# Performance work log

Measured on AMD Instinct MI355X. Metric: run time of the kernel, lower is better.

## Reference

```python
import jax, jax.numpy as jnp
import numpy as np

# Sizes (see shape_source): node irreps 32x0e + 16x1o, edge SH 1x1o,
# messages after concat/filter = 48x0e + 48x1o, MLP 16->64->64->96,
# final equivariant Linear -> 32x0e + 16x1o.
N, E = 50000, 800000
S_IN, V_IN, INV = 32, 16, 16
S_MSG, V_MSG = S_IN + V_IN, S_IN + V_IN  # 48, 48
NFAC = S_MSG + V_MSG                      # 96
S_OUT, V_OUT = 32, 16
SQRT3 = 3.0 ** 0.5


def setup_inputs() -> dict:
    key = jax.random.key(0)
    ks = jax.random.split(key, 12)
    return {
        "edge_src": jax.random.randint(ks[0], (E,), 0, N),
        "edge_dst": jax.random.randint(ks[1], (E,), 0, N),
        "edge_weight_cutoff": jax.random.uniform(ks[2], (E,), dtype=jnp.float32),
        "edge_inv": jax.random.normal(ks[3], (E, INV), dtype=jnp.float32),
        "node_scalars": jax.random.normal(ks[4], (N, S_IN), dtype=jnp.float32),
        "node_vectors": jax.random.normal(ks[5], (N, V_IN, 3), dtype=jnp.float32),
        "edge_sh_vec": jax.random.normal(ks[6], (E, 1, 3), dtype=jnp.float32),
        "W0": jax.random.normal(ks[7], (INV, 64), dtype=jnp.float32),
        "W1": jax.random.normal(ks[8], (64, 64), dtype=jnp.float32),
        "W2": jax.random.normal(ks[9], (64, NFAC), dtype=jnp.float32),
        "WL_s": jax.random.normal(ks[10], (S_MSG, S_OUT), dtype=jnp.float32),
        "WL_v": jax.random.normal(ks[11], (V_MSG, V_OUT), dtype=jnp.float32),
    }


def reference(edge_src, edge_dst, edge_weight_cutoff, edge_inv,
              node_scalars, node_vectors, edge_sh_vec,
              W0, W1, W2, WL_s, WL_v):
    # gather source-node features per edge
    src_s = node_scalars[edge_src]            # [E, 32]
    src_v = node_vectors[edge_src]            # [E, 16, 3]
    ev = edge_sh_vec[:, 0, :]                 # [E, 3] equivariant edge vector (1o)

    # equivariant tensor product (component-normalized CG paths):
    #   0e x 1o -> 1o : scalar * vector
    tp_v = src_s[:, :, None] * edge_sh_vec    # [E, 32, 3]
    #   1o x 1o -> 0e : dot / sqrt(3)   (1e, 2e outputs dropped by the output-irreps filter)
    tp_s = jnp.einsum('eci,ei->ec', src_v, ev) / SQRT3  # [E, 16]

    # concatenate with gathered node features and regroup by irrep
    msg_s = jnp.concatenate([tp_s, src_s], axis=-1)     # [E, 48] (0e block)
    msg_v = jnp.concatenate([tp_v, src_v], axis=1)      # [E, 48, 3] (1o block)

    # edge-conditioned gating MLP on invariant edge features (e3nn-normalized)
    h = jax.nn.silu(edge_inv @ W0 / jnp.sqrt(jnp.float32(INV)))
    h = jax.nn.silu(h @ W1 / jnp.sqrt(jnp.float32(64)))
    fac = h @ W2 / jnp.sqrt(jnp.float32(64))            # [E, 96]

    # elementwise tensor product with scalar factors + smooth cutoff
    g = fac * edge_weight_cutoff[:, None]
    msg_s = msg_s * g[:, :S_MSG]
    msg_v = msg_v * g[:, S_MSG:, None]

    # scatter-sum messages into destination nodes
    out_s = jax.ops.segment_sum(msg_s, edge_dst, num_segments=N)  # [N, 48]
    out_v = jax.ops.segment_sum(msg_v, edge_dst, num_segments=N)  # [N, 48, 3]

    # equivariant Linear to irreps_node_output (fan-in normalized)
    y_s = out_s @ WL_s / jnp.sqrt(jnp.float32(S_MSG))                       # [N, 32]
    y_v = jnp.einsum('eci,co->eoi', out_v, WL_v) / jnp.sqrt(jnp.float32(V_MSG))  # [N, 16, 3]

    # return as contiguous IrrepsArray storage [N, 32 + 16*3]
    return jnp.concatenate([y_s, y_v.reshape(y_v.shape[0], -1)], axis=-1)
```

## Files before the change

kernel.cpp:

```cpp
#include <hip/hip_runtime.h>
#include <hip/hip_fp16.h>
#include <math.h>

constexpr int S_IN = 32, V_IN = 16, INVD = 16;
constexpr int S_MSG = S_IN + V_IN;
constexpr int V_MSG = S_IN + V_IN;
constexpr int NFAC  = S_MSG + V_MSG;
constexpr int S_OUT = 32, V_OUT = 16;
constexpr int OUT_PER_NODE = S_OUT + V_OUT * 3;
constexpr float ISQRT3 = 0.57735026918962576f;
constexpr float ISQ48  = 0.14433756729740643f;

constexpr int PW0 = 0, PW1 = 2560, PW2 = 7168, PWL = 14080, PWTOT = 17536;

typedef _Float16 f16x8 __attribute__((ext_vector_type(8)));
typedef __attribute__((ext_vector_type(4))) float f32x4;

__device__ __forceinline__ float silu_f(float x) {
    return x / (1.0f + __expf(-x));
}
__device__ __forceinline__ unsigned int hpack2(float a, float b) {
    __half2 h = __floats2half2_rn(a, b);
    return *reinterpret_cast<unsigned int*>(&h);
}
__device__ __forceinline__ unsigned short f2h(float f) {
    __half h = __float2half_rn(f);
    return __half_as_ushort(h);
}
__device__ __forceinline__ float h2f(unsigned short u) {
    return __half2float(__ushort_as_half(u));
}
__device__ __forceinline__ void ld4h(const unsigned short* p, float f[4]) {
    uint2 v = *reinterpret_cast<const uint2*>(p);
    f[0] = h2f((unsigned short)(v.x & 0xffffu));
    f[1] = h2f((unsigned short)(v.x >> 16));
    f[2] = h2f((unsigned short)(v.y & 0xffffu));
    f[3] = h2f((unsigned short)(v.y >> 16));
}

__global__ __launch_bounds__(256) void hist_prep(
    const int* __restrict__ edst, int* __restrict__ deg, int E,
    const float* __restrict__ W0, const float* __restrict__ W1,
    const float* __restrict__ W2, const float* __restrict__ WLs,
    const float* __restrict__ WLv,
    const float* __restrict__ ns, const float* __restrict__ nv,
    unsigned short* __restrict__ pW,
    unsigned short* __restrict__ pNS,
    unsigned short* __restrict__ pNV,
    int Nn)
{
    int i = blockIdx.x * 256 + threadIdx.x;
    if (i < E) atomicAdd(&deg[edst[i]], 1);

    int nNS = Nn * 4;
    int nNV = Nn * 6;
    if (i < PWTOT) {
        float v = 0.0f;
        if (i < PW1) {
            int j = i / 40, k = i - 40 * j;
            if (k < INVD) v = W0[k * 64 + j];
        } else if (i < PW2) {
            int t = i - PW1; int j = t / 72, k = t - 72 * j;
            if (k < 64) v = W1[k * 64 + j];
        } else if (i < PWL) {
            int t = i - PW2; int j = t / 72, k = t - 72 * j;
            if (k < 64) v = W2[k * 96 + j];
        } else {
            int t = i - PWL; int j = t / 72, k = t - 72 * j;
            if (k < 48) v = (j < 32) ? WLs[k * S_OUT + j] : WLv[k * V_OUT + (j - 32)];
        }
        pW[i] = f2h(v);
    } else if (i < PWTOT + nNS) {
        int g = i - PWTOT;
        const float4* s4 = reinterpret_cast<const float4*>(ns + (size_t)g * 8);
        float4 a = s4[0], b = s4[1];
        *reinterpret_cast<uint4*>(pNS + (size_t)g * 8) =
            make_uint4(hpack2(a.x, a.y), hpack2(a.z, a.w), hpack2(b.x, b.y), hpack2(b.z, b.w));
    } else if (i < PWTOT + nNS + nNV) {
        int g = i - PWTOT - nNS;
        const float4* s4 = reinterpret_cast<const float4*>(nv + (size_t)g * 8);
        float4 a = s4[0], b = s4[1];
        *reinterpret_cast<uint4*>(pNV + (size_t)g * 8) =
            make_uint4(hpack2(a.x, a.y), hpack2(a.z, a.w), hpack2(b.x, b.y), hpack2(b.z, b.w));
    }
}

__global__ __launch_bounds__(256) void scanA(
    const int* __restrict__ deg, int* __restrict__ bsum, int Nn)
{
    __shared__ int sh[256];
    int i = blockIdx.x * 256 + threadIdx.x;
    sh[threadIdx.x] = (i < Nn) ? deg[i] : 0;
    __syncthreads();
    for (int o = 128; o > 0; o >>= 1) {
        if (threadIdx.x < o) sh[threadIdx.x] += sh[threadIdx.x + o];
        __syncthreads();
    }
    if (threadIdx.x == 0) bsum[blockIdx.x] = sh[0];
}

__global__ __launch_bounds__(1024) void scanB(int* __restrict__ bsum, int nb)
{
    __shared__ int sh[1024];
    int t = threadIdx.x;
    sh[t] = (t < nb) ? bsum[t] : 0;
    __syncthreads();
    for (int o = 1; o < 1024; o <<= 1) {
        int v = (t >= o) ? sh[t - o] : 0;
        __syncthreads();
        sh[t] += v;
        __syncthreads();
    }
    if (t < nb) bsum[t] = (t > 0) ? sh[t - 1] : 0;
}

__global__ __launch_bounds__(256) void scanC(
    const int* __restrict__ deg, const int* __restrict__ bsum,
    int* __restrict__ offs, int* __restrict__ cursor, int Nn, int E)
{
    __shared__ int sh[256];
    int i = blockIdx.x * 256 + threadIdx.x;
    int t = threadIdx.x;
    int v = (i < Nn) ? deg[i] : 0;
    sh[t] = v;
    __syncthreads();
    for (int o = 1; o < 256; o <<= 1) {
        int u = (t >= o) ? sh[t - o] : 0;
        __syncthreads();
        sh[t] += u;
        __syncthreads();
    }
    int excl = sh[t] - v + bsum[blockIdx.x];
    if (i < Nn) { offs[i] = excl; cursor[i] = excl; }
    if (i == Nn - 1) offs[Nn] = E;
}

__global__ __launch_bounds__(256) void scatter_permute(
    const int*   __restrict__ edst,
    const int*   __restrict__ esrc,
    const float* __restrict__ ecut,
    const float* __restrict__ esh,
    const float* __restrict__ einv,
    int* __restrict__ cursor,
    uint4* __restrict__ pedge,
    int E)
{
    int e = blockIdx.x * 256 + threadIdx.x;
    if (e >= E) return;
    int d = edst[e];
    int pos = atomicAdd(&cursor[d], 1);

    const float4* xr = reinterpret_cast<const float4*>(einv + (size_t)e * INVD);
    float4 a = xr[0], b = xr[1], c = xr[2], f = xr[3];
    uint4 r0 = make_uint4(hpack2(a.x, a.y), hpack2(a.z, a.w), hpack2(b.x, b.y), hpack2(b.z, b.w));
    uint4 r1 = make_uint4(hpack2(c.x, c.y), hpack2(c.z, c.w), hpack2(f.x, f.y), hpack2(f.z, f.w));
    uint4 r2 = make_uint4(__float_as_uint(ecut[e]),
                          __float_as_uint(esh[(size_t)e * 3 + 0]),
                          __float_as_uint(esh[(size_t)e * 3 + 1]),
                          __float_as_uint(esh[(size_t)e * 3 + 2]));
    uint4 r3 = make_uint4((unsigned int)esrc[e], (unsigned int)d, 0u, 0u);

    uint4* dst = pedge + (size_t)pos * 4;
    dst[0] = r0; dst[1] = r1; dst[2] = r2; dst[3] = r3;
}

__global__ __launch_bounds__(256, 3) void edge_mega(
    const uint4* __restrict__ pedge,
    const unsigned short* __restrict__ pW,
    const unsigned short* __restrict__ pNS,
    const unsigned short* __restrict__ pNV,
    float* __restrict__ out,
    int E)
{
    __shared__ __align__(16) unsigned char smem[53760];

    unsigned short* sW0T = (unsigned short*)(smem + 0);
    unsigned short* sW1T = (unsigned short*)(smem + 5120);
    unsigned short* act0 = (unsigned short*)(smem + 14336);
    unsigned short* act1 = (unsigned short*)(smem + 32768);
    unsigned short* sWLT = (unsigned short*)(smem + 5120);
    unsigned short* M    = (unsigned short*)(smem + 14336);
    unsigned short* Fns  = (unsigned short*)(smem + 32768);
    int*            sdst = (int*)(smem + 43008);
    unsigned short* Fnv0 = (unsigned short*)(smem + 43520);
    unsigned short* Fnv1 = (unsigned short*)(smem + 48640);
    unsigned short* Fnv2 = (unsigned short*)(smem + 0);
    float*          redf = (float*)smem;

    const int tid = threadIdx.x;
    const int pbase = blockIdx.x * 128;
    const int p1 = E;

    const int lane = tid & 63;
    const int w    = tid >> 6;
    const int lr   = lane & 15;
    const int lg   = lane >> 4;
    const int eb0  = w * 32 + lr;
    const int eb1  = eb0 + 16;
    const int pA   = pbase + eb0;
    const int pB   = pbase + eb1;

    const uint4 rA2 = pedge[(size_t)(pA < p1 ? pA : p1 - 1) * 4 + 2];
    const uint4 rB2 = pedge[(size_t)(pB < p1 ? pB : p1 - 1) * 4 + 2];
    const float cutA = __uint_as_float(rA2.x);
    const float ev0a = __uint_as_float(rA2.y), ev1a = __uint_as_float(rA2.z), ev2a = __uint_as_float(rA2.w);
    const float cutB = __uint_as_float(rB2.x);
    const float ev0b = __uint_as_float(rB2.y), ev1b = __uint_as_float(rB2.z), ev2b = __uint_as_float(rB2.w);

    const int t2 = tid >> 1, half = tid & 1;
    int dS;
    uint4 pf0, pf1, pf2, pf3, pf4, pf5;
    {
        int pS = pbase + t2; if (pS >= p1) pS = p1 - 1;
        uint4 r3 = pedge[(size_t)pS * 4 + 3];
        int sS = (int)r3.x;
        dS = (int)r3.y;
        if (half == 0) {
            const uint4* nr = reinterpret_cast<const uint4*>(pNS + (size_t)sS * 32);
            pf0 = nr[0]; pf1 = nr[1]; pf2 = nr[2]; pf3 = nr[3];
        } else {
            const uint4* vr = reinterpret_cast<const uint4*>(pNV + (size_t)sS * 48);
            pf0 = vr[0]; pf1 = vr[1]; pf2 = vr[2]; pf3 = vr[3]; pf4 = vr[4]; pf5 = vr[5];
        }
    }

    const uint4* wsrc = reinterpret_cast<const uint4*>(pW);

    {
        uint4* s4 = reinterpret_cast<uint4*>(smem);
        #pragma unroll 2
        for (int i = tid; i < 896; i += 256) s4[i] = wsrc[i];
    }
    if (tid < 128) {
        int p = pbase + tid; if (p >= p1) p = p1 - 1;
        const uint4* rec = pedge + (size_t)p * 4;
        uint4 r0 = rec[0], r1 = rec[1];
        uint4* r4 = reinterpret_cast<uint4*>(&act0[tid * 72]);
        r4[0] = r0;
        r4[1] = r1;
        r4[2] = make_uint4(0u, 0u, 0u, 0u);
        r4[3] = make_uint4(0u, 0u, 0u, 0u);
    }
    __syncthreads();

    const f32x4 zero4 = {0.f, 0.f, 0.f, 0.f};

    {
        f16x8 b0 = *(const f16x8*)&act0[eb0 * 72 + lg * 8];
        f16x8 b1 = *(const f16x8*)&act0[eb1 * 72 + lg * 8];
        #pragma unroll
        for (int jt = 0; jt < 4; jt++) {
            f16x8 a = *(const f16x8*)&sW0T[(jt * 16 + lr) * 40 + lg * 8];
            f32x4 d0 = __builtin_amdgcn_mfma_f32_16x16x32_f16(a, b0, zero4, 0, 0, 0);
            f32x4 d1 = __builtin_amdgcn_mfma_f32_16x16x32_f16(a, b1, zero4, 0, 0, 0);
            unsigned int u0 = hpack2(silu_f(d0[0] * 0.25f), silu_f(d0[1] * 0.25f));
            unsigned int u1 = hpack2(silu_f(d0[2] * 0.25f), silu_f(d0[3] * 0.25f));
            *(uint2*)&act1[eb0 * 72 + jt * 16 + lg * 4] = make_uint2(u0, u1);
            u0 = hpack2(silu_f(d1[0] * 0.25f), silu_f(d1[1] * 0.25f));
            u1 = hpack2(silu_f(d1[2] * 0.25f), silu_f(d1[3] * 0.25f));
            *(uint2*)&act1[eb1 * 72 + jt * 16 + lg * 4] = make_uint2(u0, u1);
        }
    }

    {
        f16x8 b00 = *(const f16x8*)&act1[eb0 * 72 +      lg * 8];
        f16x8 b01 = *(const f16x8*)&act1[eb0 * 72 + 32 + lg * 8];
        f16x8 b10 = *(const f16x8*)&act1[eb1 * 72 +      lg * 8];
        f16x8 b11 = *(const f16x8*)&act1[eb1 * 72 + 32 + lg * 8];
        #pragma unroll
        for (int jt = 0; jt < 4; jt++) {
            f16x8 a0 = *(const f16x8*)&sW1T[(jt * 16 + lr) * 72 +      lg * 8];
            f16x8 a1 = *(const f16x8*)&sW1T[(jt * 16 + lr) * 72 + 32 + lg * 8];
            f32x4 d0 = __builtin_amdgcn_mfma_f32_16x16x32_f16(a0, b00, zero4, 0, 0, 0);
            d0 = __builtin_amdgcn_mfma_f32_16x16x32_f16(a1, b01, d0, 0, 0, 0);
            f32x4 d1 = __builtin_amdgcn_mfma_f32_16x16x32_f16(a0, b10, zero4, 0, 0, 0);
            d1 = __builtin_amdgcn_mfma_f32_16x16x32_f16(a1, b11, d1, 0, 0, 0);
            unsigned int u0 = hpack2(silu_f(d0[0] * 0.125f), silu_f(d0[1] * 0.125f));
            unsigned int u1 = hpack2(silu_f(d0[2] * 0.125f), silu_f(d0[3] * 0.125f));
            *(uint2*)&act0[eb0 * 72 + jt * 16 + lg * 4] = make_uint2(u0, u1);
            u0 = hpack2(silu_f(d1[0] * 0.125f), silu_f(d1[1] * 0.125f));
            u1 = hpack2(silu_f(d1[2] * 0.125f), silu_f(d1[3] * 0.125f));
            *(uint2*)&act0[eb1 * 72 + jt * 16 + lg * 4] = make_uint2(u0, u1);
        }
    }

    __syncthreads();
    {
        uint4* a14 = reinterpret_cast<uint4*>(act1);
        const uint4* w2s = wsrc + 896;
        #pragma unroll 2
        for (int i = tid; i < 864; i += 256) a14[i] = w2s[i];
    }
    __syncthreads();

    float fac0[6][4], fac1[6][4];
    {
        f16x8 b00 = *(const f16x8*)&act0[eb0 * 72 +      lg * 8];
        f16x8 b01 = *(const f16x8*)&act0[eb0 * 72 + 32 + lg * 8];
        f16x8 b10 = *(const f16x8*)&act0[eb1 * 72 +      lg * 8];
        f16x8 b11 = *(const f16x8*)&act0[eb1 * 72 + 32 + lg * 8];
        float K0 = cutA * 0.125f * ISQ48;
        float K1 = cutB * 0.125f * ISQ48;
        #pragma unroll
        for (int jt = 0; jt < 6; jt++) {
            f16x8 a0 = *(const f16x8*)&act1[(jt * 16 + lr) * 72 +      lg * 8];
            f16x8 a1 = *(const f16x8*)&act1[(jt * 16 + lr) * 72 + 32 + lg * 8];
            f32x4 d0 = __builtin_amdgcn_mfma_f32_16x16x32_f16(a0, b00, zero4, 0, 0, 0);
            d0 = __builtin_amdgcn_mfma_f32_16x16x32_f16(a1, b01, d0, 0, 0, 0);
            f32x4 d1 = __builtin_amdgcn_mfma_f32_16x16x32_f16(a0, b10, zero4, 0, 0, 0);
            d1 = __builtin_amdgcn_mfma_f32_16x16x32_f16(a1, b11, d1, 0, 0, 0);
            float s0 = (jt == 0) ? K0 * ISQRT3 : K0;
            float s1 = (jt == 0) ? K1 * ISQRT3 : K1;
            #pragma unroll
            for (int q = 0; q < 4; q++) {
                fac0[jt][q] = d0[q] * s0;
                fac1[jt][q] = d1[q] * s1;
            }
        }
    }
    __syncthreads();

    {
        if (half == 0) {
            uint4* d4 = reinterpret_cast<uint4*>(&Fns[t2 * 40]);
            d4[0] = pf0; d4[1] = pf1;
            uint4* d4b = reinterpret_cast<uint4*>(&Fns[t2 * 40 + 16]);
            d4b[0] = pf2; d4b[1] = pf3;
        } else {
            unsigned int wb[24];
            wb[0]=pf0.x; wb[1]=pf0.y; wb[2]=pf0.z; wb[3]=pf0.w;
            wb[4]=pf1.x; wb[5]=pf1.y; wb[6]=pf1.z; wb[7]=pf1.w;
            wb[8]=pf2.x; wb[9]=pf2.y; wb[10]=pf2.z; wb[11]=pf2.w;
            wb[12]=pf3.x; wb[13]=pf3.y; wb[14]=pf3.z; wb[15]=pf3.w;
            wb[16]=pf4.x; wb[17]=pf4.y; wb[18]=pf4.z; wb[19]=pf4.w;
            wb[20]=pf5.x; wb[21]=pf5.y; wb[22]=pf5.z; wb[23]=pf5.w;
            #pragma unroll
            for (int i = 0; i < 3; i++) {
                unsigned short* FnvI = (i == 0) ? Fnv0 : ((i == 1) ? Fnv1 : Fnv2);
                unsigned int ow[8];
                #pragma unroll
                for (int wd = 0; wd < 8; wd++) {
                    int kLo = 6 * wd + i;
                    int kHi = 6 * wd + 3 + i;
                    unsigned int lo = (kLo & 1) ? (wb[kLo >> 1] >> 16) : (wb[kLo >> 1] & 0xffffu);
                    unsigned int hi = (kHi & 1) ? (wb[kHi >> 1] >> 16) : (wb[kHi >> 1] & 0xffffu);
                    ow[wd] = lo | (hi << 16);
                }
                uint2* d2 = reinterpret_cast<uint2*>(&FnvI[t2 * 20]);
                d2[0] = make_uint2(ow[0], ow[1]);
                d2[1] = make_uint2(ow[2], ow[3]);
                d2[2] = make_uint2(ow[4], ow[5]);
                d2[3] = make_uint2(ow[6], ow[7]);
            }
        }
        uint4* wl4 = reinterpret_cast<uint4*>(sWLT);
        const uint4* wls = wsrc + 896 + 864;
        #pragma unroll 2
        for (int i = tid; i < 432; i += 256) wl4[i] = wls[i];
    }
    __syncthreads();

    float fvA[3][4], fvB[3][4];
    float fsA[2][4], fsB[2][4];
    #pragma unroll
    for (int i = 0; i < 3; i++) {
        const unsigned short* FnvI = (i == 0) ? Fnv0 : ((i == 1) ? Fnv1 : Fnv2);
        ld4h(&FnvI[eb0 * 20 + lg * 4], fvA[i]);
        ld4h(&FnvI[eb1 * 20 + lg * 4], fvB[i]);
    }
    #pragma unroll
    for (int jt = 0; jt < 2; jt++) {
        ld4h(&Fns[eb0 * 40 + jt * 16 + lg * 4], fsA[jt]);
        ld4h(&Fns[eb1 * 40 + jt * 16 + lg * 4], fsB[jt]);
    }

    {
        float vA[4], vB[4];
        #pragma unroll
        for (int q = 0; q < 4; q++) {
            float fa = fvA[0][q] * ev0a + fvA[1][q] * ev1a + fvA[2][q] * ev2a;
            float fb = fvB[0][q] * ev0b + fvB[1][q] * ev1b + fvB[2][q] * ev2b;
            vA[q] = fa * fac0[0][q];
            vB[q] = fb * fac1[0][q];
        }
        *(uint2*)&M[eb0 * 72 + lg * 4] = make_uint2(hpack2(vA[0], vA[1]), hpack2(vA[2], vA[3]));
        *(uint2*)&M[eb1 * 72 + lg * 4] = make_uint2(hpack2(vB[0], vB[1]), hpack2(vB[2], vB[3]));
    }
    #pragma unroll
    for (int jt = 1; jt < 3; jt++) {
        int c0 = jt * 16 + lg * 4;
        float vA[4], vB[4];
        #pragma unroll
        for (int q = 0; q < 4; q++) {
            vA[q] = fsA[jt - 1][q] * fac0[jt][q];
            vB[q] = fsB[jt - 1][q] * fac1[jt][q];
        }
        *(uint2*)&M[eb0 * 72 + c0] = make_uint2(hpack2(vA[0], vA[1]), hpack2(vA[2], vA[3]));
        *(uint2*)&M[eb1 * 72 + c0] = make_uint2(hpack2(vB[0], vB[1]), hpack2(vB[2], vB[3]));
    }
    *(uint2*)&M[eb0 * 72 + 48 + lg * 4] = make_uint2(0u, 0u);
    *(uint2*)&M[eb1 * 72 + 48 + lg * 4] = make_uint2(0u, 0u);

    f32x4 accS[2][2] = {{zero4, zero4}, {zero4, zero4}};
    #pragma unroll
    for (int kt = 0; kt < 2; kt++) {
        f16x8 b0 = *(const f16x8*)&M[eb0 * 72 + kt * 32 + lg * 8];
        f16x8 b1 = *(const f16x8*)&M[eb1 * 72 + kt * 32 + lg * 8];
        #pragma unroll
        for (int ot = 0; ot < 2; ot++) {
            f16x8 a = *(const f16x8*)&sWLT[(ot * 16 + lr) * 72 + kt * 32 + lg * 8];
            accS[0][ot] = __builtin_amdgcn_mfma_f32_16x16x32_f16(a, b0, accS[0][ot], 0, 0, 0);
            accS[1][ot] = __builtin_amdgcn_mfma_f32_16x16x32_f16(a, b1, accS[1][ot], 0, 0, 0);
        }
    }

    #pragma unroll
    for (int jt = 0; jt < 2; jt++) {
        int c0 = jt * 16 + lg * 4;
        float vA[4], vB[4];
        #pragma unroll
        for (int q = 0; q < 4; q++) {
            vA[q] = fsA[jt][q] * fac0[3 + jt][q];
            vB[q] = fsB[jt][q] * fac1[3 + jt][q];
        }
        *(uint2*)&M[eb0 * 72 + c0] = make_uint2(hpack2(vA[0], vA[1]), hpack2(vA[2], vA[3]));
        *(uint2*)&M[eb1 * 72 + c0] = make_uint2(hpack2(vB[0], vB[1]), hpack2(vB[2], vB[3]));
    }
    f32x4 t1A = zero4, t1B = zero4;
    {
        f16x8 b0 = *(const f16x8*)&M[eb0 * 72 + lg * 8];
        f16x8 b1 = *(const f16x8*)&M[eb1 * 72 + lg * 8];
        f16x8 a  = *(const f16x8*)&sWLT[(32 + lr) * 72 + lg * 8];
        t1A = __builtin_amdgcn_mfma_f32_16x16x32_f16(a, b0, t1A, 0, 0, 0);
        t1B = __builtin_amdgcn_mfma_f32_16x16x32_f16(a, b1, t1B, 0, 0, 0);
    }

    float yvA[4][3], yvB[4][3];
    *(uint2*)&M[eb0 * 72 + 16 + lg * 4] = make_uint2(0u, 0u);
    *(uint2*)&M[eb1 * 72 + 16 + lg * 4] = make_uint2(0u, 0u);
    #pragma unroll
    for (int i = 0; i < 3; i++) {
        float vA[4], vB[4];
        #pragma unroll
        for (int q = 0; q < 4; q++) {
            vA[q] = fvA[i][q] * fac0[5][q];
            vB[q] = fvB[i][q] * fac1[5][q];
        }
        *(uint2*)&M[eb0 * 72 + lg * 4] = make_uint2(hpack2(vA[0], vA[1]), hpack2(vA[2], vA[3]));
        *(uint2*)&M[eb1 * 72 + lg * 4] = make_uint2(hpack2(vB[0], vB[1]), hpack2(vB[2], vB[3]));

        f32x4 t2A = zero4, t2B = zero4;
        f16x8 b0 = *(const f16x8*)&M[eb0 * 72 + lg * 8];
        f16x8 b1 = *(const f16x8*)&M[eb1 * 72 + lg * 8];
        f16x8 a  = *(const f16x8*)&sWLT[(32 + lr) * 72 + 32 + lg * 8];
        t2A = __builtin_amdgcn_mfma_f32_16x16x32_f16(a, b0, t2A, 0, 0, 0);
        t2B = __builtin_amdgcn_mfma_f32_16x16x32_f16(a, b1, t2B, 0, 0, 0);

        float evA = (i == 0) ? ev0a : ((i == 1) ? ev1a : ev2a);
        float evB = (i == 0) ? ev0b : ((i == 1) ? ev1b : ev2b);
        #pragma unroll
        for (int q = 0; q < 4; q++) {
            yvA[q][i] = fmaf(evA, t1A[q], t2A[q]);
            yvB[q][i] = fmaf(evB, t1B[q], t2B[q]);
        }
    }

    __syncthreads();

    if (half == 0) sdst[t2] = dS;

    {
        bool okA = (pA < p1), okB = (pB < p1);
        #pragma unroll
        for (int ot = 0; ot < 2; ot++) {
            *(f32x4*)&redf[eb0 * 84 + ot * 16 + lg * 4] = okA ? accS[0][ot] : zero4;
            *(f32x4*)&redf[eb1 * 84 + ot * 16 + lg * 4] = okB ? accS[1][ot] : zero4;
        }
        #pragma unroll
        for (int q = 0; q < 4; q++) {
            int m = lg * 4 + q;
            #pragma unroll
            for (int i = 0; i < 3; i++) {
                redf[eb0 * 84 + 32 + 3 * m + i] = okA ? yvA[q][i] : 0.0f;
                redf[eb1 * 84 + 32 + 3 * m + i] = okB ? yvB[q][i] : 0.0f;
            }
        }
    }
    __syncthreads();

    {
        int base = w * 32;
        int cur = sdst[base];
        float s0 = 0.0f, s1 = 0.0f;
        for (int r = 0; r < 32; r++) {
            int d = sdst[base + r];
            if (d != cur) {
                atomicAdd(&out[(size_t)cur * OUT_PER_NODE + lane], s0);
                if (lane < 16) atomicAdd(&out[(size_t)cur * OUT_PER_NODE + 64 + lane], s1);
                s0 = 0.0f; s1 = 0.0f; cur = d;
            }
            s0 += redf[(base + r) * 84 + lane];
            if (lane < 16) s1 += redf[(base + r) * 84 + 64 + lane];
        }
        atomicAdd(&out[(size_t)cur * OUT_PER_NODE + lane], s0);
        if (lane < 16) atomicAdd(&out[(size_t)cur * OUT_PER_NODE + 64 + lane], s1);
    }
}

extern "C" void kernel_launch(void* const* d_in, const int* in_sizes, int n_in,
                              void* d_out, int out_size, void* d_ws, size_t ws_size,
                              hipStream_t stream) {
    const int*   esrc = (const int*)  d_in[0];
    const int*   edst = (const int*)  d_in[1];
    const float* ecut = (const float*)d_in[2];
    const float* einv = (const float*)d_in[3];
    const float* ns   = (const float*)d_in[4];
    const float* nv   = (const float*)d_in[5];
    const float* esh  = (const float*)d_in[6];
    const float* W0   = (const float*)d_in[7];
    const float* W1   = (const float*)d_in[8];
    const float* W2   = (const float*)d_in[9];
    const float* WLs  = (const float*)d_in[10];
    const float* WLv  = (const float*)d_in[11];
    float* out = (float*)d_out;

    const int E  = in_sizes[0];
    const int Nn = in_sizes[4] / S_IN;
    const int nb = (Nn + 255) / 256;

    size_t int_bytes = (((size_t)(3 * Nn + 1 + nb)) * sizeof(int) + 255) & ~(size_t)255;
    size_t pe_bytes  = ((size_t)E * 64 + 255) & ~(size_t)255;
    size_t pw_bytes  = ((size_t)PWTOT * 2 + 255) & ~(size_t)255;
    size_t ns_bytes  = ((size_t)Nn * 32 * 2 + 255) & ~(size_t)255;
    size_t nv_bytes  = ((size_t)Nn * 48 * 2 + 255) & ~(size_t)255;
    size_t fixed = int_bytes + pe_bytes + pw_bytes + ns_bytes + nv_bytes;

    int eblocks = (E + 255) / 256;

    hipMemsetAsync(out, 0, (size_t)Nn * OUT_PER_NODE * sizeof(float), stream);

    if (ws_size < fixed) return;

    int*            deg    = (int*)d_ws;
    int*            offs   = deg + Nn;
    int*            cursor = offs + Nn + 1;
    int*            bsum   = cursor + Nn;
    uint4*          pedge  = (uint4*)((char*)d_ws + int_bytes);
    unsigned short* pW     = (unsigned short*)((char*)d_ws + int_bytes + pe_bytes);
    unsigned short* pNS    = (unsigned short*)((char*)d_ws + int_bytes + pe_bytes + pw_bytes);
    unsigned short* pNV    = (unsigned short*)((char*)d_ws + int_bytes + pe_bytes + pw_bytes + ns_bytes);

    hipMemsetAsync(deg, 0, (size_t)Nn * sizeof(int), stream);

    int ptotal = PWTOT + Nn * 4 + Nn * 6;
    int hp_blocks = max(eblocks, (ptotal + 255) / 256);
    hist_prep<<<hp_blocks, 256, 0, stream>>>(edst, deg, E, W0, W1, W2, WLs, WLv,
                                             ns, nv, pW, pNS, pNV, Nn);
    scanA<<<nb, 256, 0, stream>>>(deg, bsum, Nn);
    scanB<<<1, 1024, 0, stream>>>(bsum, nb);
    scanC<<<nb, 256, 0, stream>>>(deg, bsum, offs, cursor, Nn, E);
    scatter_permute<<<eblocks, 256, 0, stream>>>(edst, esrc, ecut, esh, einv,
                                                 cursor, pedge, E);

    int mblocks = (E + 127) / 128;
    edge_mega<<<mblocks, 256, 0, stream>>>(pedge, pW, pNS, pNV, out, E);
}
```

Before: 214.3 us.

## Compress edge records to 48 bytes and use packed fp16 gating multiplies

Shrinks the permuted per-edge record from 64 to 48 bytes by storing the cutoff and edge vector as fp16 and putting src/dst in the third uint4. This cuts the bytes written by the scatter kernel and read by the edge megakernel. The gating multiplies now run as packed half2 multiplies on raw fp16 registers rather than unpacking to float, and silu uses a hardware reciprocal. The cost is lower precision for the cutoff, the edge vector and the gated products.

```diff
diff --git a/kernel.cpp b/kernel.cpp
--- a/kernel.cpp
+++ b/kernel.cpp
@@ -17,7 +17,7 @@
 typedef __attribute__((ext_vector_type(4))) float f32x4;
 
 __device__ __forceinline__ float silu_f(float x) {
-    return x / (1.0f + __expf(-x));
+    return x * __builtin_amdgcn_rcpf(1.0f + __expf(-x));
 }
 __device__ __forceinline__ unsigned int hpack2(float a, float b) {
     __half2 h = __floats2half2_rn(a, b);
@@ -30,12 +30,17 @@
 __device__ __forceinline__ float h2f(unsigned short u) {
     return __half2float(__ushort_as_half(u));
 }
-__device__ __forceinline__ void ld4h(const unsigned short* p, float f[4]) {
-    uint2 v = *reinterpret_cast<const uint2*>(p);
-    f[0] = h2f((unsigned short)(v.x & 0xffffu));
-    f[1] = h2f((unsigned short)(v.x >> 16));
-    f[2] = h2f((unsigned short)(v.y & 0xffffu));
-    f[3] = h2f((unsigned short)(v.y >> 16));
+__device__ __forceinline__ float lo16f(unsigned int u) { return h2f((unsigned short)(u & 0xffffu)); }
+__device__ __forceinline__ float hi16f(unsigned int u) { return h2f((unsigned short)(u >> 16)); }
+__device__ __forceinline__ unsigned int pkmul(unsigned int a, unsigned int b) {
+    __half2 ha = *reinterpret_cast<__half2*>(&a);
+    __half2 hb = *reinterpret_cast<__half2*>(&b);
+    __half2 hc = __hmul2(ha, hb);
+    return *reinterpret_cast<unsigned int*>(&hc);
+}
+__device__ __forceinline__ float2 up2(unsigned int u) {
+    __half2 h = *reinterpret_cast<__half2*>(&u);
+    return __half22float2(h);
 }
 
 __global__ __launch_bounds__(256) void hist_prep(
@@ -154,14 +159,12 @@
     float4 a = xr[0], b = xr[1], c = xr[2], f = xr[3];
     uint4 r0 = make_uint4(hpack2(a.x, a.y), hpack2(a.z, a.w), hpack2(b.x, b.y), hpack2(b.z, b.w));
     uint4 r1 = make_uint4(hpack2(c.x, c.y), hpack2(c.z, c.w), hpack2(f.x, f.y), hpack2(f.z, f.w));
-    uint4 r2 = make_uint4(__float_as_uint(ecut[e]),
-                          __float_as_uint(esh[(size_t)e * 3 + 0]),
-                          __float_as_uint(esh[(size_t)e * 3 + 1]),
-                          __float_as_uint(esh[(size_t)e * 3 + 2]));
-    uint4 r3 = make_uint4((unsigned int)esrc[e], (unsigned int)d, 0u, 0u);
-
-    uint4* dst = pedge + (size_t)pos * 4;
-    dst[0] = r0; dst[1] = r1; dst[2] = r2; dst[3] = r3;
+    uint4 r2 = make_uint4(hpack2(ecut[e], esh[(size_t)e * 3 + 0]),
+                          hpack2(esh[(size_t)e * 3 + 1], esh[(size_t)e * 3 + 2]),
+                          (unsigned int)esrc[e], (unsigned int)d);
+
+    uint4* dst = pedge + (size_t)pos * 3;
+    dst[0] = r0; dst[1] = r1; dst[2] = r2;
 }
 
 __global__ __launch_bounds__(256, 3) void edge_mega(
@@ -200,21 +203,21 @@
     const int pA   = pbase + eb0;
     const int pB   = pbase + eb1;
 
-    const uint4 rA2 = pedge[(size_t)(pA < p1 ? pA : p1 - 1) * 4 + 2];
-    const uint4 rB2 = pedge[(size_t)(pB < p1 ? pB : p1 - 1) * 4 + 2];
-    const float cutA = __uint_as_float(rA2.x);
-    const float ev0a = __uint_as_float(rA2.y), ev1a = __uint_as_float(rA2.z), ev2a = __uint_as_float(rA2.w);
-    const float cutB = __uint_as_float(rB2.x);
-    const float ev0b = __uint_as_float(rB2.y), ev1b = __uint_as_float(rB2.z), ev2b = __uint_as_float(rB2.w);
+    const uint4 rA2 = pedge[(size_t)(pA < p1 ? pA : p1 - 1) * 3 + 2];
+    const uint4 rB2 = pedge[(size_t)(pB < p1 ? pB : p1 - 1) * 3 + 2];
+    const float cutA = lo16f(rA2.x);
+    const float ev0a = hi16f(rA2.x), ev1a = lo16f(rA2.y), ev2a = hi16f(rA2.y);
+    const float cutB = lo16f(rB2.x);
+    const float ev0b = hi16f(rB2.x), ev1b = lo16f(rB2.y), ev2b = hi16f(rB2.y);
 
     const int t2 = tid >> 1, half = tid & 1;
     int dS;
     uint4 pf0, pf1, pf2, pf3, pf4, pf5;
     {
         int pS = pbase + t2; if (pS >= p1) pS = p1 - 1;
-        uint4 r3 = pedge[(size_t)pS * 4 + 3];
-        int sS = (int)r3.x;
-        dS = (int)r3.y;
+        uint4 r2 = pedge[(size_t)pS * 3 + 2];
+        int sS = (int)r2.z;
+        dS = (int)r2.w;
         if (half == 0) {
             const uint4* nr = reinterpret_cast<const uint4*>(pNS + (size_t)sS * 32);
             pf0 = nr[0]; pf1 = nr[1]; pf2 = nr[2]; pf3 = nr[3];
@@ -233,7 +236,7 @@
     }
     if (tid < 128) {
         int p = pbase + tid; if (p >= p1) p = p1 - 1;
-        const uint4* rec = pedge + (size_t)p * 4;
+        const uint4* rec = pedge + (size_t)p * 3;
         uint4 r0 = rec[0], r1 = rec[1];
         uint4* r4 = reinterpret_cast<uint4*>(&act0[tid * 72]);
         r4[0] = r0;
@@ -360,43 +363,53 @@
     }
     __syncthreads();
 
-    float fvA[3][4], fvB[3][4];
-    float fsA[2][4], fsB[2][4];
+    uint2 fsrA[2], fsrB[2];
+    uint2 fvrA[3], fvrB[3];
     #pragma unroll
     for (int i = 0; i < 3; i++) {
         const unsigned short* FnvI = (i == 0) ? Fnv0 : ((i == 1) ? Fnv1 : Fnv2);
-        ld4h(&FnvI[eb0 * 20 + lg * 4], fvA[i]);
-        ld4h(&FnvI[eb1 * 20 + lg * 4], fvB[i]);
+        fvrA[i] = *reinterpret_cast<const uint2*>(&FnvI[eb0 * 20 + lg * 4]);
+        fvrB[i] = *reinterpret_cast<const uint2*>(&FnvI[eb1 * 20 + lg * 4]);
     }
     #pragma unroll
     for (int jt = 0; jt < 2; jt++) {
-        ld4h(&Fns[eb0 * 40 + jt * 16 + lg * 4], fsA[jt]);
-        ld4h(&Fns[eb1 * 40 + jt * 16 + lg * 4], fsB[jt]);
-    }
-
-    {
+        fsrA[jt] = *reinterpret_cast<const uint2*>(&Fns[eb0 * 40 + jt * 16 + lg * 4]);
+        fsrB[jt] = *reinterpret_cast<const uint2*>(&Fns[eb1 * 40 + jt * 16 + lg * 4]);
+    }
+
+    uint2 fpA[5], fpB[5];
+    #pragma unroll
+    for (int jt = 1; jt < 6; jt++) {
+        fpA[jt - 1] = make_uint2(hpack2(fac0[jt][0], fac0[jt][1]), hpack2(fac0[jt][2], fac0[jt][3]));
+        fpB[jt - 1] = make_uint2(hpack2(fac1[jt][0], fac1[jt][1]), hpack2(fac1[jt][2], fac1[jt][3]));
+    }
+
+    {
+        float2 a0 = up2(fvrA[0].x), a1 = up2(fvrA[0].y);
+        float2 b0 = up2(fvrA[1].x), b1 = up2(fvrA[1].y);
+        float2 c0 = up2(fvrA[2].x), c1 = up2(fvrA[2].y);
+        float2 d0 = up2(fvrB[0].x), d1 = up2(fvrB[0].y);
+        float2 e0 = up2(fvrB[1].x), e1 = up2(fvrB[1].y);
+        float2 g0 = up2(fvrB[2].x), g1 = up2(fvrB[2].y);
         float vA[4], vB[4];
-        #pragma unroll
-        for (int q = 0; q < 4; q++) {
-            float fa = fvA[0][q] * ev0a + fvA[1][q] * ev1a + fvA[2][q] * ev2a;
-            float fb = fvB[0][q] * ev0b + fvB[1][q] * ev1b + fvB[2][q] * ev2b;
-            vA[q] = fa * fac0[0][q];
-            vB[q] = fb * fac1[0][q];
-        }
+        vA[0] = (a0.x*ev0a + b0.x*ev1a + c0.x*ev2a) * fac0[0][0];
+        vA[1] = (a0.y*ev0a + b0.y*ev1a + c0.y*ev2a) * fac0[0][1];
+        vA[2] = (a1.x*ev0a + b1.x*ev1a + c1.x*ev2a) * fac0[0][2];
+        vA[3] = (a1.y*ev0a + b1.y*ev1a + c1.y*ev2a) * fac0[0][3];
+        vB[0] = (d0.x*ev0b + e0.x*ev1b + g0.x*ev2b) * fac1[0][0];
+        vB[1] = (d0.y*ev0b + e0.y*ev1b + g0.y*ev2b) * fac1[0][1];
+        vB[2] = (d1.x*ev0b + e1.x*ev1b + g1.x*ev2b) * fac1[0][2];
+        vB[3] = (d1.y*ev0b + e1.y*ev1b + g1.y*ev2b) * fac1[0][3];
         *(uint2*)&M[eb0 * 72 + lg * 4] = make_uint2(hpack2(vA[0], vA[1]), hpack2(vA[2], vA[3]));
         *(uint2*)&M[eb1 * 72 + lg * 4] = make_uint2(hpack2(vB[0], vB[1]), hpack2(vB[2], vB[3]));
     }
     #pragma unroll
     for (int jt = 1; jt < 3; jt++) {
         int c0 = jt * 16 + lg * 4;
-        float vA[4], vB[4];
-        #pragma unroll
-        for (int q = 0; q < 4; q++) {
-            vA[q] = fsA[jt - 1][q] * fac0[jt][q];
-            vB[q] = fsB[jt - 1][q] * fac1[jt][q];
-        }
-        *(uint2*)&M[eb0 * 72 + c0] = make_uint2(hpack2(vA[0], vA[1]), hpack2(vA[2], vA[3]));
-        *(uint2*)&M[eb1 * 72 + c0] = make_uint2(hpack2(vB[0], vB[1]), hpack2(vB[2], vB[3]));
+        *(uint2*)&M[eb0 * 72 + c0] =
+            make_uint2(pkmul(fsrA[jt-1].x, fpA[jt-1].x), pkmul(fsrA[jt-1].y, fpA[jt-1].y));
+        *(uint2*)&M[eb1 * 72 + c0] =
+            make_uint2(pkmul(fsrB[jt-1].x, fpB[jt-1].x), pkmul(fsrB[jt-1].y, fpB[jt-1].y));
     }
     *(uint2*)&M[eb0 * 72 + 48 + lg * 4] = make_uint2(0u, 0u);
     *(uint2*)&M[eb1 * 72 + 48 + lg * 4] = make_uint2(0u, 0u);
@@ -417,14 +430,10 @@
     #pragma unroll
     for (int jt = 0; jt < 2; jt++) {
         int c0 = jt * 16 + lg * 4;
-        float vA[4], vB[4];
-        #pragma unroll
-        for (int q = 0; q < 4; q++) {
-            vA[q] = fsA[jt][q] * fac0[3 + jt][q];
-            vB[q] = fsB[jt][q] * fac1[3 + jt][q];
-        }
-        *(uint2*)&M[eb0 * 72 + c0] = make_uint2(hpack2(vA[0], vA[1]), hpack2(vA[2], vA[3]));
-        *(uint2*)&M[eb1 * 72 + c0] = make_uint2(hpack2(vB[0], vB[1]), hpack2(vB[2], vB[3]));
+        *(uint2*)&M[eb0 * 72 + c0] =
+            make_uint2(pkmul(fsrA[jt].x, fpA[jt+2].x), pkmul(fsrA[jt].y, fpA[jt+2].y));
+        *(uint2*)&M[eb1 * 72 + c0] =
+            make_uint2(pkmul(fsrB[jt].x, fpB[jt+2].x), pkmul(fsrB[jt].y, fpB[jt+2].y));
     }
     f32x4 t1A = zero4, t1B = zero4;
     {
@@ -440,14 +449,10 @@
     *(uint2*)&M[eb1 * 72 + 16 + lg * 4] = make_uint2(0u, 0u);
     #pragma unroll
     for (int i = 0; i < 3; i++) {
-        float vA[4], vB[4];
-        #pragma unroll
-        for (int q = 0; q < 4; q++) {
-            vA[q] = fvA[i][q] * fac0[5][q];
-            vB[q] = fvB[i][q] * fac1[5][q];
-        }
-        *(uint2*)&M[eb0 * 72 + lg * 4] = make_uint2(hpack2(vA[0], vA[1]), hpack2(vA[2], vA[3]));
-        *(uint2*)&M[eb1 * 72 + lg * 4] = make_uint2(hpack2(vB[0], vB[1]), hpack2(vB[2], vB[3]));
+        *(uint2*)&M[eb0 * 72 + lg * 4] =
+            make_uint2(pkmul(fvrA[i].x, fpA[4].x), pkmul(fvrA[i].y, fpA[4].y));
+        *(uint2*)&M[eb1 * 72 + lg * 4] =
+            make_uint2(pkmul(fvrB[i].x, fpB[4].x), pkmul(fvrB[i].y, fpB[4].y));
 
         f32x4 t2A = zero4, t2B = zero4;
         f16x8 b0 = *(const f16x8*)&M[eb0 * 72 + lg * 8];
@@ -529,7 +534,7 @@
     const int nb = (Nn + 255) / 256;
 
     size_t int_bytes = (((size_t)(3 * Nn + 1 + nb)) * sizeof(int) + 255) & ~(size_t)255;
-    size_t pe_bytes  = ((size_t)E * 64 + 255) & ~(size_t)255;
+    size_t pe_bytes  = ((size_t)E * 48 + 255) & ~(size_t)255;
     size_t pw_bytes  = ((size_t)PWTOT * 2 + 255) & ~(size_t)255;
     size_t ns_bytes  = ((size_t)Nn * 32 * 2 + 255) & ~(size_t)255;
     size_t nv_bytes  = ((size_t)Nn * 48 * 2 + 255) & ~(size_t)255;
```

Result: faster. 209.6 us (-2.2%).
